# Performance work log

Measured on AMD Instinct MI355X. Metric: run time of the kernel, lower is better.

## Reference

```python
import jax, jax.numpy as jnp
import numpy as np

BN_EPS = 1e-5


def setup_inputs() -> dict:
    key = jax.random.key(0)
    k1, k2, k3, k4 = jax.random.split(key, 4)
    B, C_in, T, V = 64, 64, 300, 25
    K, C_out = 3, 64
    x = jax.random.normal(k1, (B, C_in, T, V), dtype=jnp.float32)
    # 1x1 Conv2d weight collapsed to (K*C_out, C_in); bias (K*C_out,)
    W = jax.random.normal(k2, (K * C_out, C_in), dtype=jnp.float32) * (1.0 / np.sqrt(C_in))
    b = jax.random.normal(k3, (K * C_out,), dtype=jnp.float32) * 0.02
    A = jax.random.uniform(k4, (K, V, V), dtype=jnp.float32)
    gamma = jnp.ones((C_out,), dtype=jnp.float32)
    beta = jnp.zeros((C_out,), dtype=jnp.float32)
    return {"x": x, "W": W, "b": b, "A": A, "gamma": gamma, "beta": beta}


def reference(x, W, b, A, gamma, beta):
    B, C_in, T, V = x.shape
    K = A.shape[0]
    C_out = W.shape[0] // K
    # 1x1 conv == per-pixel matmul over channels
    x_conv = jnp.einsum('bctv,oc->botv', x, W) + b[None, :, None, None]
    # split into K partitions: (B, K, C_out, T, V)
    x_conv = x_conv.reshape(B, K, C_out, T, V)
    # fused per-partition graph matmul + sum over partitions
    out = jnp.einsum('bkctv,kvw->bctw', x_conv, A)
    # BatchNorm2d (training mode: batch statistics over B, T, V)
    mean = jnp.mean(out, axis=(0, 2, 3), keepdims=True)
    var = jnp.var(out, axis=(0, 2, 3), keepdims=True)  # biased variance
    out_hat = (out - mean) * jax.lax.rsqrt(var + BN_EPS)
    return out_hat * gamma[None, :, None, None] + beta[None, :, None, None]
```

## Files before the change

kernel.cpp:

```cpp
#include <hip/hip_runtime.h>
#include <stdint.h>


#define TT 3
#define NPIX (TT * 25)
#define NT1 5
#define NBLK 6400

typedef short bf16x8 __attribute__((ext_vector_type(8)));
typedef float f32x4 __attribute__((ext_vector_type(4)));

union frag_u { bf16x8 v; uint32_t u[4]; };

__device__ inline short f2bf(float f) {
    union { float f; uint32_t u; } v; v.f = f;
    uint32_t u = v.u;
    u += 0x7fffu + ((u >> 16) & 1u);
    return (short)(u >> 16);
}

__device__ inline uint32_t cvtpk(float lo, float hi) {
    uint32_t d;
    asm("v_cvt_pk_bf16_f32 %0, %1, %2" : "=v"(d) : "v"(lo), "v"(hi));
    return d;
}

__global__ __launch_bounds__(256, 3) void sgc_main(
    const float* __restrict__ x, const float* __restrict__ W,
    const float* __restrict__ bias, const float* __restrict__ A,
    float* __restrict__ out, float* __restrict__ stats_part)
{
    __shared__ __align__(16) short Ylds[18432];
    __shared__ __align__(16) short Acat[3072];

    const int tid  = threadIdx.x;
    const int lane = tid & 63;
    const int wave = tid >> 6;
    const int q4   = lane >> 4;
    const int wl   = lane & 15;
    const int bid  = blockIdx.x;
    const int b    = bid / 100;
    const int t0   = (bid % 100) * TT;

    {
        bf16x8 z8 = {0,0,0,0,0,0,0,0};
        #pragma unroll
        for (int j = 0; j < 3; ++j) {
            int s = tid + 256 * j;
            if (s < 576)
                *(bf16x8*)&Ylds[(s >> 4) * 512 + 384 + (s & 15) * 8] = z8;
        }
    }

    #pragma unroll
    for (int j = 0; j < 2; ++j) {
        int g = tid + 256 * j;
        if (g < 384) {
            int tile = g >> 6;
            int kb2  = tile >> 1, nt2 = tile & 1;
            int oct  = (g >> 4) & 3;
            int w    = nt2 * 16 + (g & 15);
            frag_u fr;
            #pragma unroll
            for (int p = 0; p < 4; ++p) {
                int v0 = oct * 8 + 2 * p;
                float a0 = (w < 25 && v0     < 25) ? A[(kb2 * 25 + v0) * 25 + w]     : 0.f;
                float a1 = (w < 25 && v0 + 1 < 25) ? A[(kb2 * 25 + v0 + 1) * 25 + w] : 0.f;
                fr.u[p] = cvtpk(a0, a1);
            }
            *(bf16x8*)&Acat[g * 8] = fr.v;
        }
    }

    bf16x8 wfrag[3][2];
    #pragma unroll
    for (int mti = 0; mti < 3; ++mti) {
        int o = (wave * 3 + mti) * 16 + wl;
        #pragma unroll
        for (int kb = 0; kb < 2; ++kb) {
            int ci0 = kb * 32 + q4 * 8;
            const float4 f0 = *(const float4*)&W[o * 64 + ci0];
            const float4 f1 = *(const float4*)&W[o * 64 + ci0 + 4];
            frag_u fr;
            fr.u[0] = cvtpk(f0.x, f0.y);
            fr.u[1] = cvtpk(f0.z, f0.w);
            fr.u[2] = cvtpk(f1.x, f1.y);
            fr.u[3] = cvtpk(f1.z, f1.w);
            wfrag[mti][kb] = fr.v;
        }
    }

    const float* xp = x + (size_t)b * 480000 + (size_t)t0 * 25;
    f32x4 acc[3][NT1];
    #pragma unroll
    for (int mti = 0; mti < 3; ++mti)
        #pragma unroll
        for (int nt = 0; nt < NT1; ++nt) {
            f32x4 zf = {0.f, 0.f, 0.f, 0.f};
            acc[mti][nt] = zf;
        }

    #pragma unroll
    for (int nt = 0; nt < NT1; ++nt) {
        int n = nt * 16 + wl;
        if (n > NPIX - 1) n = NPIX - 1;
        int loff = q4 * 60000 + n;
        bf16x8 xb[2];
        #pragma unroll
        for (int kb = 0; kb < 2; ++kb) {
            float xv[8];
            #pragma unroll
            for (int jj = 0; jj < 8; ++jj)
                xv[jj] = (xp + (kb * 32 + jj) * 7500)[loff];
            frag_u fr;
            #pragma unroll
            for (int p = 0; p < 4; ++p)
                fr.u[p] = cvtpk(xv[2 * p], xv[2 * p + 1]);
            xb[kb] = fr.v;
        }
        #pragma unroll
        for (int mti = 0; mti < 3; ++mti) {
            acc[mti][nt] = __builtin_amdgcn_mfma_f32_16x16x32_bf16(
                wfrag[mti][0], xb[0], acc[mti][nt], 0, 0, 0);
            acc[mti][nt] = __builtin_amdgcn_mfma_f32_16x16x32_bf16(
                wfrag[mti][1], xb[1], acc[mti][nt], 0, 0, 0);
        }
    }

    float4 bv[3];
    #pragma unroll
    for (int mti = 0; mti < 3; ++mti)
        bv[mti] = *(const float4*)&bias[(wave * 3 + mti) * 16 + q4 * 4];

    __syncthreads();

    #pragma unroll
    for (int nt = 0; nt < NT1; ++nt) {
        int n = nt * 16 + wl;
        if (n < NPIX) {
            int t = n / 25, v = n % 25;
            #pragma unroll
            for (int mti = 0; mti < 3; ++mti) {
                int wt = wave * 3 + mti;
                int k  = wt >> 2, cq = wt & 3;
                int kv = k * 32 + v;
                int sbase = ((t * 4 + cq) * 3 + k) * 512
                          + ((kv >> 3) & 3) * 128 + q4 * 32 + (kv & 7);
                const float* bp = (const float*)&bv[mti];
                #pragma unroll
                for (int r = 0; r < 4; ++r)
                    Ylds[sbase + r * 8] = f2bf(acc[mti][nt][r] + bp[r]);
            }
        }
    }
    __syncthreads();

    bf16x8 bfrag2[2][3];
    #pragma unroll
    for (int nt2 = 0; nt2 < 2; ++nt2)
        #pragma unroll
        for (int kb2 = 0; kb2 < 3; ++kb2)
            bfrag2[nt2][kb2] = *(const bf16x8*)&Acat[((kb2 * 2 + nt2) * 64 + lane) * 8];

    float ssum[4] = {0.f, 0.f, 0.f, 0.f};
    float ssq[4]  = {0.f, 0.f, 0.f, 0.f};
    const int c0 = wave * 16 + q4 * 4;

    #pragma unroll
    for (int t = 0; t < TT; ++t) {
        bf16x8 a2[3];
        #pragma unroll
        for (int kb2 = 0; kb2 < 3; ++kb2)
            a2[kb2] = *(const bf16x8*)&Ylds[(((t * 4 + wave) * 3 + kb2) * 64 + lane) * 8];

        f32x4 acc2[2];
        #pragma unroll
        for (int nt2 = 0; nt2 < 2; ++nt2) {
            f32x4 zf = {0.f, 0.f, 0.f, 0.f};
            acc2[nt2] = zf;
            #pragma unroll
            for (int kb2 = 0; kb2 < 3; ++kb2)
                acc2[nt2] = __builtin_amdgcn_mfma_f32_16x16x32_bf16(
                    a2[kb2], bfrag2[nt2][kb2], acc2[nt2], 0, 0, 0);
        }

        #pragma unroll
        for (int nt2 = 0; nt2 < 2; ++nt2) {
            int w = nt2 * 16 + wl;
            bool valid = (w < 25);
            #pragma unroll
            for (int r = 0; r < 4; ++r) {
                float val = acc2[nt2][r];
                if (valid) {
                    out[(size_t)((b * 64 + c0 + r) * 300 + t0 + t) * 25 + w] = val;
                    ssum[r] += val;
                    ssq[r]  += val * val;
                }
            }
        }
    }

    #pragma unroll
    for (int r = 0; r < 4; ++r) {
        float s = ssum[r], q = ssq[r];
        #pragma unroll
        for (int d = 1; d < 16; d <<= 1) {
            s += __shfl_xor(s, d);
            q += __shfl_xor(q, d);
        }
        if (wl == 0) {
            int c = c0 + r;
            int slot = bid & 63;
            atomicAdd(&stats_part[slot * 128 + c], s);
            atomicAdd(&stats_part[slot * 128 + 64 + c], q);
        }
    }
}

__global__ void sgc_finalize(const float* __restrict__ stats_part,
                             const float* __restrict__ gamma,
                             const float* __restrict__ beta,
                             float* __restrict__ scaleshift)
{
    int c = threadIdx.x;
    float s = 0.f, q = 0.f;
    #pragma unroll 8
    for (int slot = 0; slot < 64; ++slot) {
        s += stats_part[slot * 128 + c];
        q += stats_part[slot * 128 + 64 + c];
    }
    const float invN = 1.f / 480000.f;
    float mean = s * invN;
    float var  = q * invN - mean * mean;
    float rstd = rsqrtf(var + 1e-5f);
    float sc = rstd * gamma[c];
    scaleshift[c]      = sc;
    scaleshift[64 + c] = beta[c] - mean * sc;
}

__global__ __launch_bounds__(256) void sgc_norm(float* __restrict__ out,
                                                const float* __restrict__ scaleshift)
{
    const int total4 = 30720000 / 4;
    int stride = gridDim.x * 256;
    for (int i = blockIdx.x * 256 + threadIdx.x; i < total4; i += stride) {
        int c = (i / 1875) & 63;
        float sc = scaleshift[c], sh = scaleshift[64 + c];
        float4 v = *((float4*)out + i);
        v.x = v.x * sc + sh;
        v.y = v.y * sc + sh;
        v.z = v.z * sc + sh;
        v.w = v.w * sc + sh;
        *((float4*)out + i) = v;
    }
}

extern "C" void kernel_launch(void* const* d_in, const int* in_sizes, int n_in,
                              void* d_out, int out_size, void* d_ws, size_t ws_size,
                              hipStream_t stream)
{
    const float* x     = (const float*)d_in[0];
    const float* W     = (const float*)d_in[1];
    const float* bias  = (const float*)d_in[2];
    const float* A     = (const float*)d_in[3];
    const float* gamma = (const float*)d_in[4];
    const float* beta  = (const float*)d_in[5];
    float* out = (float*)d_out;

    float* stats      = (float*)d_ws;
    float* scaleshift = stats + 64 * 128;

    hipMemsetAsync(stats, 0, 64 * 128 * sizeof(float), stream);
    sgc_main<<<NBLK, 256, 0, stream>>>(x, W, bias, A, out, stats);
    sgc_finalize<<<1, 64, 0, stream>>>(stats, gamma, beta, scaleshift);
    sgc_norm<<<4096, 256, 0, stream>>>(out, scaleshift);
}
```

Baseline: 354.7 us.

## Stage pre-norm output as fp16 workspace tiles and normalize into output

The main kernel now processes five time sub-chunks per block and writes its pre-BatchNorm result as fp16 tiles into the workspace instead of fp32 into the output. A new normalize kernel reads those tiles and writes the final fp32 output. This avoids the read-modify-write pass over the full fp32 output, cutting global memory traffic. It trades this for an fp16 intermediate, fewer larger blocks, and a dependence on a workspace big enough to hold the tiles, with the old path kept as a fallback.

```diff
diff --git a/kernel.cpp b/kernel.cpp
--- a/kernel.cpp
+++ b/kernel.cpp
@@ -3,9 +3,13 @@
 
 
 #define TT 3
+#define NSUB 5
+#define CHT (TT * NSUB)
 #define NPIX (TT * 25)
 #define NT1 5
-#define NBLK 6400
+#define NBLK 1280
+#define TROW 376
+#define TSZ  24064
 
 typedef short bf16x8 __attribute__((ext_vector_type(8)));
 typedef float f32x4 __attribute__((ext_vector_type(4)));
@@ -25,10 +29,17 @@
     return d;
 }
 
+__device__ inline short f2h(float f) {
+    union { _Float16 h; short s; } u; u.h = (_Float16)f; return u.s;
+}
+__device__ inline float h2f(short s) {
+    union { short s; _Float16 h; } u; u.s = s; return (float)u.h;
+}
+
 __global__ __launch_bounds__(256, 3) void sgc_main(
     const float* __restrict__ x, const float* __restrict__ W,
     const float* __restrict__ bias, const float* __restrict__ A,
-    float* __restrict__ out, float* __restrict__ stats_part)
+    short* __restrict__ ws, float* __restrict__ stats_part)
 {
     __shared__ __align__(16) short Ylds[18432];
     __shared__ __align__(16) short Acat[3072];
@@ -39,8 +50,8 @@
     const int q4   = lane >> 4;
     const int wl   = lane & 15;
     const int bid  = blockIdx.x;
-    const int b    = bid / 100;
-    const int t0   = (bid % 100) * TT;
+    const int b    = bid / 20;
+    const int t0   = (bid % 20) * CHT;
 
     {
         bf16x8 z8 = {0,0,0,0,0,0,0,0};
@@ -90,69 +101,11 @@
         }
     }
 
-    const float* xp = x + (size_t)b * 480000 + (size_t)t0 * 25;
-    f32x4 acc[3][NT1];
-    #pragma unroll
-    for (int mti = 0; mti < 3; ++mti)
-        #pragma unroll
-        for (int nt = 0; nt < NT1; ++nt) {
-            f32x4 zf = {0.f, 0.f, 0.f, 0.f};
-            acc[mti][nt] = zf;
-        }
-
-    #pragma unroll
-    for (int nt = 0; nt < NT1; ++nt) {
-        int n = nt * 16 + wl;
-        if (n > NPIX - 1) n = NPIX - 1;
-        int loff = q4 * 60000 + n;
-        bf16x8 xb[2];
-        #pragma unroll
-        for (int kb = 0; kb < 2; ++kb) {
-            float xv[8];
-            #pragma unroll
-            for (int jj = 0; jj < 8; ++jj)
-                xv[jj] = (xp + (kb * 32 + jj) * 7500)[loff];
-            frag_u fr;
-            #pragma unroll
-            for (int p = 0; p < 4; ++p)
-                fr.u[p] = cvtpk(xv[2 * p], xv[2 * p + 1]);
-            xb[kb] = fr.v;
-        }
-        #pragma unroll
-        for (int mti = 0; mti < 3; ++mti) {
-            acc[mti][nt] = __builtin_amdgcn_mfma_f32_16x16x32_bf16(
-                wfrag[mti][0], xb[0], acc[mti][nt], 0, 0, 0);
-            acc[mti][nt] = __builtin_amdgcn_mfma_f32_16x16x32_bf16(
-                wfrag[mti][1], xb[1], acc[mti][nt], 0, 0, 0);
-        }
-    }
-
     float4 bv[3];
     #pragma unroll
     for (int mti = 0; mti < 3; ++mti)
         bv[mti] = *(const float4*)&bias[(wave * 3 + mti) * 16 + q4 * 4];
 
-    __syncthreads();
-
-    #pragma unroll
-    for (int nt = 0; nt < NT1; ++nt) {
-        int n = nt * 16 + wl;
-        if (n < NPIX) {
-            int t = n / 25, v = n % 25;
-            #pragma unroll
-            for (int mti = 0; mti < 3; ++mti) {
-                int wt = wave * 3 + mti;
-                int k  = wt >> 2, cq = wt & 3;
-                int kv = k * 32 + v;
-                int sbase = ((t * 4 + cq) * 3 + k) * 512
-                          + ((kv >> 3) & 3) * 128 + q4 * 32 + (kv & 7);
-                const float* bp = (const float*)&bv[mti];
-                #pragma unroll
-                for (int r = 0; r < 4; ++r)
-                    Ylds[sbase + r * 8] = f2bf(acc[mti][nt][r] + bp[r]);
-            }
-        }
-    }
     __syncthreads();
 
     bf16x8 bfrag2[2][3];
@@ -165,36 +118,100 @@
     float ssum[4] = {0.f, 0.f, 0.f, 0.f};
     float ssq[4]  = {0.f, 0.f, 0.f, 0.f};
     const int c0 = wave * 16 + q4 * 4;
-
-    #pragma unroll
-    for (int t = 0; t < TT; ++t) {
-        bf16x8 a2[3];
-        #pragma unroll
-        for (int kb2 = 0; kb2 < 3; ++kb2)
-            a2[kb2] = *(const bf16x8*)&Ylds[(((t * 4 + wave) * 3 + kb2) * 64 + lane) * 8];
-
-        f32x4 acc2[2];
-        #pragma unroll
-        for (int nt2 = 0; nt2 < 2; ++nt2) {
-            f32x4 zf = {0.f, 0.f, 0.f, 0.f};
-            acc2[nt2] = zf;
+    short* wstile = ws + (size_t)bid * TSZ;
+
+    for (int s = 0; s < NSUB; ++s) {
+        const float* xp = x + (size_t)b * 480000 + (size_t)(t0 + s * TT) * 25;
+        f32x4 acc[3][NT1];
+        #pragma unroll
+        for (int mti = 0; mti < 3; ++mti)
+            #pragma unroll
+            for (int nt = 0; nt < NT1; ++nt) {
+                f32x4 zf = {0.f, 0.f, 0.f, 0.f};
+                acc[mti][nt] = zf;
+            }
+
+        #pragma unroll
+        for (int nt = 0; nt < NT1; ++nt) {
+            int n = nt * 16 + wl;
+            if (n > NPIX - 1) n = NPIX - 1;
+            int loff = q4 * 60000 + n;
+            bf16x8 xb[2];
+            #pragma unroll
+            for (int kb = 0; kb < 2; ++kb) {
+                float xv[8];
+                #pragma unroll
+                for (int jj = 0; jj < 8; ++jj)
+                    xv[jj] = (xp + (kb * 32 + jj) * 7500)[loff];
+                frag_u fr;
+                #pragma unroll
+                for (int p = 0; p < 4; ++p)
+                    fr.u[p] = cvtpk(xv[2 * p], xv[2 * p + 1]);
+                xb[kb] = fr.v;
+            }
+            #pragma unroll
+            for (int mti = 0; mti < 3; ++mti) {
+                acc[mti][nt] = __builtin_amdgcn_mfma_f32_16x16x32_bf16(
+                    wfrag[mti][0], xb[0], acc[mti][nt], 0, 0, 0);
+                acc[mti][nt] = __builtin_amdgcn_mfma_f32_16x16x32_bf16(
+                    wfrag[mti][1], xb[1], acc[mti][nt], 0, 0, 0);
+            }
+        }
+
+        __syncthreads();
+
+        #pragma unroll
+        for (int nt = 0; nt < NT1; ++nt) {
+            int n = nt * 16 + wl;
+            if (n < NPIX) {
+                int t = n / 25, v = n % 25;
+                #pragma unroll
+                for (int mti = 0; mti < 3; ++mti) {
+                    int wt = wave * 3 + mti;
+                    int k  = wt >> 2, cq = wt & 3;
+                    int kv = k * 32 + v;
+                    int sbase = ((t * 4 + cq) * 3 + k) * 512
+                              + ((kv >> 3) & 3) * 128 + q4 * 32 + (kv & 7);
+                    const float* bp = (const float*)&bv[mti];
+                    #pragma unroll
+                    for (int r = 0; r < 4; ++r)
+                        Ylds[sbase + r * 8] = f2bf(acc[mti][nt][r] + bp[r]);
+                }
+            }
+        }
+        __syncthreads();
+
+        #pragma unroll
+        for (int t = 0; t < TT; ++t) {
+            bf16x8 a2[3];
             #pragma unroll
             for (int kb2 = 0; kb2 < 3; ++kb2)
-                acc2[nt2] = __builtin_amdgcn_mfma_f32_16x16x32_bf16(
-                    a2[kb2], bfrag2[nt2][kb2], acc2[nt2], 0, 0, 0);
-        }
-
-        #pragma unroll
-        for (int nt2 = 0; nt2 < 2; ++nt2) {
-            int w = nt2 * 16 + wl;
-            bool valid = (w < 25);
-            #pragma unroll
-            for (int r = 0; r < 4; ++r) {
-                float val = acc2[nt2][r];
-                if (valid) {
-                    out[(size_t)((b * 64 + c0 + r) * 300 + t0 + t) * 25 + w] = val;
-                    ssum[r] += val;
-                    ssq[r]  += val * val;
+                a2[kb2] = *(const bf16x8*)&Ylds[(((t * 4 + wave) * 3 + kb2) * 64 + lane) * 8];
+
+            f32x4 acc2[2];
+            #pragma unroll
+            for (int nt2 = 0; nt2 < 2; ++nt2) {
+                f32x4 zf = {0.f, 0.f, 0.f, 0.f};
+                acc2[nt2] = zf;
+                #pragma unroll
+                for (int kb2 = 0; kb2 < 3; ++kb2)
+                    acc2[nt2] = __builtin_amdgcn_mfma_f32_16x16x32_bf16(
+                        a2[kb2], bfrag2[nt2][kb2], acc2[nt2], 0, 0, 0);
+            }
+
+            int tloc = s * TT + t;
+            #pragma unroll
+            for (int nt2 = 0; nt2 < 2; ++nt2) {
+                int w = nt2 * 16 + wl;
+                bool valid = (w < 25);
+                #pragma unroll
+                for (int r = 0; r < 4; ++r) {
+                    float val = acc2[nt2][r];
+                    if (valid) {
+                        wstile[(c0 + r) * TROW + tloc * 25 + w] = f2h(val);
+                        ssum[r] += val;
+                        ssq[r]  += val * val;
+                    }
                 }
             }
         }
@@ -238,8 +255,227 @@
     scaleshift[64 + c] = beta[c] - mean * sc;
 }
 
-__global__ __launch_bounds__(256) void sgc_norm(float* __restrict__ out,
-                                                const float* __restrict__ scaleshift)
+__global__ __launch_bounds__(256) void sgc_normws(
+    const short* __restrict__ ws, const float* __restrict__ scaleshift,
+    float* __restrict__ out)
+{
+    const int tid = threadIdx.x;
+    const int bid = blockIdx.x;
+    const int b   = bid / 20;
+    const int chunk = bid % 20;
+    const short* tile = ws + (size_t)bid * TSZ;
+    float* obase = out + (size_t)b * 480000 + (size_t)chunk * (CHT * 25);
+
+    int i = tid;
+    #pragma unroll 3
+    for (int j = 0; j < 93; ++j, i += 256) {
+        int c = i / 375;
+        int rem = i - c * 375;
+        float y = h2f(tile[c * TROW + rem]);
+        obase[c * 7500 + rem] = y * scaleshift[c] + scaleshift[64 + c];
+    }
+    if (i < 24000) {
+        int c = i / 375;
+        int rem = i - c * 375;
+        float y = h2f(tile[c * TROW + rem]);
+        obase[c * 7500 + rem] = y * scaleshift[c] + scaleshift[64 + c];
+    }
+}
+
+__global__ __launch_bounds__(256, 3) void sgc_main_fb(
+    const float* __restrict__ x, const float* __restrict__ W,
+    const float* __restrict__ bias, const float* __restrict__ A,
+    float* __restrict__ out, float* __restrict__ stats_part)
+{
+    __shared__ __align__(16) short Ylds[18432];
+    __shared__ __align__(16) short Acat[3072];
+
+    const int tid  = threadIdx.x;
+    const int lane = tid & 63;
+    const int wave = tid >> 6;
+    const int q4   = lane >> 4;
+    const int wl   = lane & 15;
+    const int bid  = blockIdx.x;
+    const int b    = bid / 100;
+    const int t0   = (bid % 100) * TT;
+
+    {
+        bf16x8 z8 = {0,0,0,0,0,0,0,0};
+        #pragma unroll
+        for (int j = 0; j < 3; ++j) {
+            int s = tid + 256 * j;
+            if (s < 576)
+                *(bf16x8*)&Ylds[(s >> 4) * 512 + 384 + (s & 15) * 8] = z8;
+        }
+    }
+
+    #pragma unroll
+    for (int j = 0; j < 2; ++j) {
+        int g = tid + 256 * j;
+        if (g < 384) {
+            int tile = g >> 6;
+            int kb2  = tile >> 1, nt2 = tile & 1;
+            int oct  = (g >> 4) & 3;
+            int w    = nt2 * 16 + (g & 15);
+            frag_u fr;
+            #pragma unroll
+            for (int p = 0; p < 4; ++p) {
+                int v0 = oct * 8 + 2 * p;
+                float a0 = (w < 25 && v0     < 25) ? A[(kb2 * 25 + v0) * 25 + w]     : 0.f;
+                float a1 = (w < 25 && v0 + 1 < 25) ? A[(kb2 * 25 + v0 + 1) * 25 + w] : 0.f;
+                fr.u[p] = cvtpk(a0, a1);
+            }
+            *(bf16x8*)&Acat[g * 8] = fr.v;
+        }
+    }
+
+    bf16x8 wfrag[3][2];
+    #pragma unroll
+    for (int mti = 0; mti < 3; ++mti) {
+        int o = (wave * 3 + mti) * 16 + wl;
+        #pragma unroll
+        for (int kb = 0; kb < 2; ++kb) {
+            int ci0 = kb * 32 + q4 * 8;
+            const float4 f0 = *(const float4*)&W[o * 64 + ci0];
+            const float4 f1 = *(const float4*)&W[o * 64 + ci0 + 4];
+            frag_u fr;
+            fr.u[0] = cvtpk(f0.x, f0.y);
+            fr.u[1] = cvtpk(f0.z, f0.w);
+            fr.u[2] = cvtpk(f1.x, f1.y);
+            fr.u[3] = cvtpk(f1.z, f1.w);
+            wfrag[mti][kb] = fr.v;
+        }
+    }
+
+    const float* xp = x + (size_t)b * 480000 + (size_t)t0 * 25;
+    f32x4 acc[3][NT1];
+    #pragma unroll
+    for (int mti = 0; mti < 3; ++mti)
+        #pragma unroll
+        for (int nt = 0; nt < NT1; ++nt) {
+            f32x4 zf = {0.f, 0.f, 0.f, 0.f};
+            acc[mti][nt] = zf;
+        }
+
+    #pragma unroll
+    for (int nt = 0; nt < NT1; ++nt) {
+        int n = nt * 16 + wl;
+        if (n > NPIX - 1) n = NPIX - 1;
+        int loff = q4 * 60000 + n;
+        bf16x8 xb[2];
+        #pragma unroll
+        for (int kb = 0; kb < 2; ++kb) {
+            float xv[8];
+            #pragma unroll
+            for (int jj = 0; jj < 8; ++jj)
+                xv[jj] = (xp + (kb * 32 + jj) * 7500)[loff];
+            frag_u fr;
+            #pragma unroll
+            for (int p = 0; p < 4; ++p)
+                fr.u[p] = cvtpk(xv[2 * p], xv[2 * p + 1]);
+            xb[kb] = fr.v;
+        }
+        #pragma unroll
+        for (int mti = 0; mti < 3; ++mti) {
+            acc[mti][nt] = __builtin_amdgcn_mfma_f32_16x16x32_bf16(
+                wfrag[mti][0], xb[0], acc[mti][nt], 0, 0, 0);
+            acc[mti][nt] = __builtin_amdgcn_mfma_f32_16x16x32_bf16(
+                wfrag[mti][1], xb[1], acc[mti][nt], 0, 0, 0);
+        }
+    }
+
+    float4 bv[3];
+    #pragma unroll
+    for (int mti = 0; mti < 3; ++mti)
+        bv[mti] = *(const float4*)&bias[(wave * 3 + mti) * 16 + q4 * 4];
+
+    __syncthreads();
+
+    #pragma unroll
+    for (int nt = 0; nt < NT1; ++nt) {
+        int n = nt * 16 + wl;
+        if (n < NPIX) {
+            int t = n / 25, v = n % 25;
+            #pragma unroll
+            for (int mti = 0; mti < 3; ++mti) {
+                int wt = wave * 3 + mti;
+                int k  = wt >> 2, cq = wt & 3;
+                int kv = k * 32 + v;
+                int sbase = ((t * 4 + cq) * 3 + k) * 512
+                          + ((kv >> 3) & 3) * 128 + q4 * 32 + (kv & 7);
+                const float* bp = (const float*)&bv[mti];
+                #pragma unroll
+                for (int r = 0; r < 4; ++r)
+                    Ylds[sbase + r * 8] = f2bf(acc[mti][nt][r] + bp[r]);
+            }
+        }
+    }
+    __syncthreads();
+
+    bf16x8 bfrag2[2][3];
+    #pragma unroll
+    for (int nt2 = 0; nt2 < 2; ++nt2)
+        #pragma unroll
+        for (int kb2 = 0; kb2 < 3; ++kb2)
+            bfrag2[nt2][kb2] = *(const bf16x8*)&Acat[((kb2 * 2 + nt2) * 64 + lane) * 8];
+
+    float ssum[4] = {0.f, 0.f, 0.f, 0.f};
+    float ssq[4]  = {0.f, 0.f, 0.f, 0.f};
+    const int c0 = wave * 16 + q4 * 4;
+
+    #pragma unroll
+    for (int t = 0; t < TT; ++t) {
+        bf16x8 a2[3];
+        #pragma unroll
+        for (int kb2 = 0; kb2 < 3; ++kb2)
+            a2[kb2] = *(const bf16x8*)&Ylds[(((t * 4 + wave) * 3 + kb2) * 64 + lane) * 8];
+
+        f32x4 acc2[2];
+        #pragma unroll
+        for (int nt2 = 0; nt2 < 2; ++nt2) {
+            f32x4 zf = {0.f, 0.f, 0.f, 0.f};
+            acc2[nt2] = zf;
+            #pragma unroll
+            for (int kb2 = 0; kb2 < 3; ++kb2)
+                acc2[nt2] = __builtin_amdgcn_mfma_f32_16x16x32_bf16(
+                    a2[kb2], bfrag2[nt2][kb2], acc2[nt2], 0, 0, 0);
+        }
+
+        #pragma unroll
+        for (int nt2 = 0; nt2 < 2; ++nt2) {
+            int w = nt2 * 16 + wl;
+            bool valid = (w < 25);
+            #pragma unroll
+            for (int r = 0; r < 4; ++r) {
+                float val = acc2[nt2][r];
+                if (valid) {
+                    out[(size_t)((b * 64 + c0 + r) * 300 + t0 + t) * 25 + w] = val;
+                    ssum[r] += val;
+                    ssq[r]  += val * val;
+                }
+            }
+        }
+    }
+
+    #pragma unroll
+    for (int r = 0; r < 4; ++r) {
+        float s = ssum[r], q = ssq[r];
+        #pragma unroll
+        for (int d = 1; d < 16; d <<= 1) {
+            s += __shfl_xor(s, d);
+            q += __shfl_xor(q, d);
+        }
+        if (wl == 0) {
+            int c = c0 + r;
+            int slot = bid & 63;
+            atomicAdd(&stats_part[slot * 128 + c], s);
+            atomicAdd(&stats_part[slot * 128 + 64 + c], q);
+        }
+    }
+}
+
+__global__ __launch_bounds__(256) void sgc_norm_fb(float* __restrict__ out,
+                                                   const float* __restrict__ scaleshift)
 {
     const int total4 = 30720000 / 4;
     int stride = gridDim.x * 256;
@@ -267,11 +503,25 @@
     const float* beta  = (const float*)d_in[5];
     float* out = (float*)d_out;
 
-    float* stats      = (float*)d_ws;
-    float* scaleshift = stats + 64 * 128;
-
-    hipMemsetAsync(stats, 0, 64 * 128 * sizeof(float), stream);
-    sgc_main<<<NBLK, 256, 0, stream>>>(x, W, bias, A, out, stats);
-    sgc_finalize<<<1, 64, 0, stream>>>(stats, gamma, beta, scaleshift);
-    sgc_norm<<<4096, 256, 0, stream>>>(out, scaleshift);
-}
+    const size_t tile_bytes = (size_t)NBLK * TSZ * sizeof(short);
+    const size_t need = tile_bytes + 64 * 128 * sizeof(float) + 128 * sizeof(float);
+
+    if (ws_size >= need) {
+        short* tiles      = (short*)d_ws;
+        float* stats      = (float*)((char*)d_ws + tile_bytes);
+        float* scaleshift = stats + 64 * 128;
+
+        hipMemsetAsync(stats, 0, 64 * 128 * sizeof(float), stream);
+        sgc_main<<<NBLK, 256, 0, stream>>>(x, W, bias, A, tiles, stats);
+        sgc_finalize<<<1, 64, 0, stream>>>(stats, gamma, beta, scaleshift);
+        sgc_normws<<<NBLK, 256, 0, stream>>>(tiles, scaleshift, out);
+    } else {
+        float* stats      = (float*)d_ws;
+        float* scaleshift = stats + 64 * 128;
+
+        hipMemsetAsync(stats, 0, 64 * 128 * sizeof(float), stream);
+        sgc_main_fb<<<6400, 256, 0, stream>>>(x, W, bias, A, out, stats);
+        sgc_finalize<<<1, 64, 0, stream>>>(stats, gamma, beta, scaleshift);
+        sgc_norm_fb<<<4096, 256, 0, stream>>>(out, scaleshift);
+    }
+}
```

Measured after the change: 482.4 us. +36.0%, slower.
